# Kernel optimization log

Hardware: AMD Instinct MI355X
Metric: run time of the kernel (lower is better)

## Reference

```python
import jax, jax.numpy as jnp
import numpy as np

M, N_GRID, DIM = 32, 32, 128
N_SAMPLES = 100000


def setup_inputs() -> dict:
    key = jax.random.key(0)
    k1, k2 = jax.random.split(key)
    x = jax.random.normal(k1, (N_SAMPLES, DIM), dtype=jnp.float32)
    som_weights = jax.random.normal(k2, (M, N_GRID, DIM), dtype=jnp.float32)
    return {"x": x, "som_weights": som_weights}


def reference(x, som_weights):
    # MiniSom.activation_response([v]) puts a 1 at the best-matching unit
    # (argmin Euclidean distance over the m*n prototype grid), then flattens.
    # Batched equivalent: [N, K] squared distances -> argmin -> one-hot.
    K = som_weights.shape[0] * som_weights.shape[1]
    w = som_weights.reshape(K, -1)                       # [K, dim]
    x_sq = jnp.sum(x * x, axis=1, keepdims=True)         # [N, 1]
    w_sq = jnp.sum(w * w, axis=1)                        # [K]
    # squared Euclidean distance; argmin identical to argmin of true distance
    d2 = x_sq + w_sq[None, :] - 2.0 * (x @ w.T)          # [N, K]
    bmu = jnp.argmin(d2, axis=1)                         # [N]
    return jax.nn.one_hot(bmu, K, dtype=jnp.float32)     # [N, K]
```

## Files before the change

kernel.cpp:

```cpp
#include <hip/hip_runtime.h>


typedef __attribute__((ext_vector_type(8))) short bf16x8;
typedef __attribute__((ext_vector_type(4))) float f32x4;

#define SOM_K 1024
#define SOM_D 128
#define MARGIN 0.02f
#define FLAG_CAP 8192

#define WS_WSQ   64
#define WS_W3    8192
#define WS_FLAGS 532480

static __device__ __forceinline__ unsigned short f2bf(float f) {
    unsigned u = __float_as_uint(f);
    return (unsigned short)((u + 0x7FFFu + ((u >> 16) & 1u)) >> 16);
}
static __device__ __forceinline__ float bf2f(unsigned short h) {
    return __uint_as_float(((unsigned)h) << 16);
}

__global__ __launch_bounds__(256) void som_prep(
    const float* __restrict__ w, unsigned short* __restrict__ w3,
    float* __restrict__ wsq, int* __restrict__ flag_count)
{
    __shared__ float ws_[16][SOM_D];
    const int nt = blockIdx.x;
    const int tid = threadIdx.x;

    if (nt == 0 && tid == 0) *flag_count = 0;

    const float* src = w + (size_t)nt * 16 * SOM_D;
    #pragma unroll
    for (int r = 0; r < 8; ++r) {
        const int e = r * 256 + tid;
        ws_[e >> 7][e & 127] = src[e];
    }
    __syncthreads();

    unsigned short* dst = w3 + (size_t)nt * 4096;
    #pragma unroll
    for (int r = 0; r < 2; ++r) {
        const int G = r * 256 + tid;
        const int s = G >> 6;
        const int l = G & 63;
        const int c = l & 15, q = l >> 4;
        bf16x8 v;
        #pragma unroll
        for (int j = 0; j < 8; ++j) {
            const int kk = 32 * s + 8 * q + j;
            const int d = kk & 127;
            const float f = ws_[c][d];
            const unsigned short h = f2bf(f);
            v[j] = (short)((kk & 128) ? f2bf(f - bf2f(h)) : h);
        }
        *(bf16x8*)(dst + G * 8) = v;
    }

    if (tid < 16) {
        double s = 0.0;
        #pragma unroll 16
        for (int d = 0; d < SOM_D; ++d) {
            double v = (double)ws_[tid][d];
            s += v * v;
        }
        wsq[nt * 16 + tid] = (float)s;
    }
}

__global__ __launch_bounds__(256) void som_main(
    const float* __restrict__ x,
    const unsigned short* __restrict__ w3,
    const float* __restrict__ wsq,
    float* __restrict__ out,
    int* __restrict__ flag_count,
    int* __restrict__ flag_list,
    int n_samples)
{
    const int lane = threadIdx.x & 63;
    const int wv   = threadIdx.x >> 6;
    const int c = lane & 15;
    const int q = lane >> 4;
    const int R0 = blockIdx.x * 64 + wv * 16;

    bf16x8 ah[4], al[4];
    {
        int row = R0 + c;
        if (row >= n_samples) row = n_samples - 1;
        const float* xp = x + (size_t)row * SOM_D + 8 * q;
        #pragma unroll
        for (int s = 0; s < 4; ++s) {
            float4 v0 = *(const float4*)(xp + 32 * s);
            float4 v1 = *(const float4*)(xp + 32 * s + 4);
            float xv[8] = {v0.x, v0.y, v0.z, v0.w, v1.x, v1.y, v1.z, v1.w};
            bf16x8 hh, ll;
            #pragma unroll
            for (int j = 0; j < 8; ++j) {
                unsigned short h = f2bf(xv[j]);
                hh[j] = (short)h;
                ll[j] = (short)f2bf(xv[j] - bf2f(h));
            }
            ah[s] = hh; al[s] = ll;
        }
    }

    float best[4], sec[4];
    int bk[4];
    #pragma unroll
    for (int r = 0; r < 4; ++r) { best[r] = 1e30f; sec[r] = 1e30f; bk[r] = 0; }

    const unsigned short* wbase = w3 + lane * 8;

    #pragma unroll 1
    for (int nt = 0; nt < 64; ++nt) {
        const int n0 = nt * 16;
        const unsigned short* wp = wbase + (size_t)nt * 4096;
        bf16x8 b[8];
        #pragma unroll
        for (int s = 0; s < 8; ++s) b[s] = *(const bf16x8*)(wp + 512 * s);
        const float wq = wsq[n0 + c];

        f32x4 aA = {0.f, 0.f, 0.f, 0.f}, aB = {0.f, 0.f, 0.f, 0.f};
        #pragma unroll
        for (int s = 0; s < 4; ++s)
            aA = __builtin_amdgcn_mfma_f32_16x16x32_bf16(ah[s], b[s], aA, 0, 0, 0);
        #pragma unroll
        for (int s = 0; s < 4; ++s)
            aA = __builtin_amdgcn_mfma_f32_16x16x32_bf16(ah[s], b[4 + s], aA, 0, 0, 0);
        #pragma unroll
        for (int s = 0; s < 4; ++s)
            aB = __builtin_amdgcn_mfma_f32_16x16x32_bf16(al[s], b[s], aB, 0, 0, 0);

        #pragma unroll
        for (int r = 0; r < 4; ++r) {
            float s0 = wq - 2.f * (aA[r] + aB[r]);
            if (s0 < best[r]) { sec[r] = best[r]; best[r] = s0; bk[r] = n0 + c; }
            else if (s0 < sec[r]) sec[r] = s0;
        }
    }

    #pragma unroll
    for (int r = 0; r < 4; ++r) {
        float b0v = best[r], s0v = sec[r];
        int k0 = bk[r];
        #pragma unroll
        for (int m = 1; m < 16; m <<= 1) {
            float ob = __shfl_xor(b0v, m);
            float os = __shfl_xor(s0v, m);
            int   ok = __shfl_xor(k0, m);
            if (ob < b0v || (ob == b0v && ok < k0)) {
                s0v = fminf(b0v, os); b0v = ob; k0 = ok;
            } else {
                s0v = fminf(s0v, ob);
            }
        }
        best[r] = b0v; sec[r] = s0v; bk[r] = k0;
    }

    if (c == 0) {
        #pragma unroll
        for (int r = 0; r < 4; ++r) {
            const int row = R0 + 4 * q + r;
            if (row < n_samples && (sec[r] - best[r]) < MARGIN) {
                int i = atomicAdd(flag_count, 1);
                if (i < FLAG_CAP) flag_list[i] = row;
            }
        }
    }

    #pragma unroll 1
    for (int rr = 0; rr < 16; ++rr) {
        const int row = R0 + rr;
        if (row >= n_samples) break;
        const int b = __shfl(bk[rr & 3], (rr >> 2) << 4);
        f32x4* op = (f32x4*)(out + (size_t)row * SOM_K);
        #pragma unroll
        for (int j = 0; j < 4; ++j) {
            const int e = j * 64 + lane;
            f32x4 v = {0.f, 0.f, 0.f, 0.f};
            if ((b >> 2) == e) v[b & 3] = 1.0f;
            op[e] = v;
        }
    }
}

__global__ __launch_bounds__(1024) void som_pass2(
    const float* __restrict__ x,
    const float* __restrict__ w,
    float* __restrict__ out,
    const int* __restrict__ flag_count,
    const int* __restrict__ flag_list)
{
    __shared__ float xs[SOM_D];
    __shared__ double rbest[16];
    __shared__ int    rk[16];

    const int tid  = threadIdx.x;
    const int lane = tid & 63;
    const int wv   = tid >> 6;
    int cnt = *flag_count;
    if (cnt > FLAG_CAP) cnt = FLAG_CAP;

    for (int i = blockIdx.x; i < cnt; i += gridDim.x) {
        const int row = flag_list[i];
        __syncthreads();
        if (tid < SOM_D) xs[tid] = x[(size_t)row * SOM_D + tid];
        __syncthreads();

        const float* wk = w + (size_t)tid * SOM_D;
        double s0 = 0.0, s1 = 0.0;
        #pragma unroll
        for (int d = 0; d < SOM_D; d += 4) {
            float4 wv4 = *(const float4*)(wk + d);
            double w0 = (double)wv4.x, w1 = (double)wv4.y;
            double w2 = (double)wv4.z, w3 = (double)wv4.w;
            s0 += w0 * (w0 - 2.0 * (double)xs[d])     + w2 * (w2 - 2.0 * (double)xs[d + 2]);
            s1 += w1 * (w1 - 2.0 * (double)xs[d + 1]) + w3 * (w3 - 2.0 * (double)xs[d + 3]);
        }
        double sc = s0 + s1;
        int bk = tid;

        #pragma unroll
        for (int off = 32; off > 0; off >>= 1) {
            double os = __shfl_down(sc, off);
            int    ok = __shfl_down(bk, off);
            if (os < sc || (os == sc && ok < bk)) { sc = os; bk = ok; }
        }
        if (lane == 0) { rbest[wv] = sc; rk[wv] = bk; }
        __syncthreads();

        if (tid == 0) {
            double b = rbest[0]; int k0 = rk[0];
            #pragma unroll
            for (int v = 1; v < 16; ++v) {
                if (rbest[v] < b || (rbest[v] == b && rk[v] < k0)) { b = rbest[v]; k0 = rk[v]; }
            }
            rk[0] = k0;
        }
        __syncthreads();
        const int bmu = rk[0];

        out[(size_t)row * SOM_K + tid] = (tid == bmu) ? 1.0f : 0.0f;
    }
}

extern "C" void kernel_launch(void* const* d_in, const int* in_sizes, int n_in,
                              void* d_out, int out_size, void* d_ws, size_t ws_size,
                              hipStream_t stream) {
    const float* x = (const float*)d_in[0];
    const float* w = (const float*)d_in[1];
    float* out = (float*)d_out;

    const int n_samples = in_sizes[0] / SOM_D;

    char* ws = (char*)d_ws;
    int*            flag_count = (int*)ws;
    float*          wsq        = (float*)(ws + WS_WSQ);
    unsigned short* w3         = (unsigned short*)(ws + WS_W3);
    int*            flag_list  = (int*)(ws + WS_FLAGS);

    som_prep<<<64, 256, 0, stream>>>(w, w3, wsq, flag_count);
    const int grid = (n_samples + 63) / 64;
    som_main<<<grid, 256, 0, stream>>>(x, w3, wsq, out, flag_count, flag_list,
                                       n_samples);
    som_pass2<<<256, 1024, 0, stream>>>(x, w, out, flag_count, flag_list);
}
```

Measured before the change: 661.4 us.

## Split one-hot output writing into a separate streaming kernel after BMU refinement

New measurement: 652.2 us. About the same (-1.4%).

```diff
diff --git a/kernel.cpp b/kernel.cpp
--- a/kernel.cpp
+++ b/kernel.cpp
@@ -12,6 +12,7 @@
 #define WS_WSQ   64
 #define WS_W3    8192
 #define WS_FLAGS 532480
+#define WS_BMU   565248
 
 static __device__ __forceinline__ unsigned short f2bf(float f) {
     unsigned u = __float_as_uint(f);
@@ -73,7 +74,7 @@
     const float* __restrict__ x,
     const unsigned short* __restrict__ w3,
     const float* __restrict__ wsq,
-    float* __restrict__ out,
+    int* __restrict__ bmu_out,
     int* __restrict__ flag_count,
     int* __restrict__ flag_list,
     int n_samples)
@@ -162,25 +163,13 @@
         #pragma unroll
         for (int r = 0; r < 4; ++r) {
             const int row = R0 + 4 * q + r;
-            if (row < n_samples && (sec[r] - best[r]) < MARGIN) {
-                int i = atomicAdd(flag_count, 1);
-                if (i < FLAG_CAP) flag_list[i] = row;
-            }
-        }
-    }
-
-    #pragma unroll 1
-    for (int rr = 0; rr < 16; ++rr) {
-        const int row = R0 + rr;
-        if (row >= n_samples) break;
-        const int b = __shfl(bk[rr & 3], (rr >> 2) << 4);
-        f32x4* op = (f32x4*)(out + (size_t)row * SOM_K);
-        #pragma unroll
-        for (int j = 0; j < 4; ++j) {
-            const int e = j * 64 + lane;
-            f32x4 v = {0.f, 0.f, 0.f, 0.f};
-            if ((b >> 2) == e) v[b & 3] = 1.0f;
-            op[e] = v;
+            if (row < n_samples) {
+                bmu_out[row] = bk[r];
+                if ((sec[r] - best[r]) < MARGIN) {
+                    int i = atomicAdd(flag_count, 1);
+                    if (i < FLAG_CAP) flag_list[i] = row;
+                }
+            }
         }
     }
 }
@@ -188,7 +177,7 @@
 __global__ __launch_bounds__(1024) void som_pass2(
     const float* __restrict__ x,
     const float* __restrict__ w,
-    float* __restrict__ out,
+    int* __restrict__ bmu_out,
     const int* __restrict__ flag_count,
     const int* __restrict__ flag_list)
 {
@@ -236,12 +225,30 @@
             for (int v = 1; v < 16; ++v) {
                 if (rbest[v] < b || (rbest[v] == b && rk[v] < k0)) { b = rbest[v]; k0 = rk[v]; }
             }
-            rk[0] = k0;
-        }
-        __syncthreads();
-        const int bmu = rk[0];
-
-        out[(size_t)row * SOM_K + tid] = (tid == bmu) ? 1.0f : 0.0f;
+            bmu_out[row] = k0;
+        }
+        __syncthreads();
+    }
+}
+
+__global__ __launch_bounds__(256) void som_write(
+    float* __restrict__ out, const int* __restrict__ bmu, int n)
+{
+    const int lane = threadIdx.x & 63;
+    const int wv   = threadIdx.x >> 6;
+    int row = blockIdx.x * 4 + wv;
+    const int stride = gridDim.x * 4;
+
+    for (; row < n; row += stride) {
+        const int b = bmu[row];
+        f32x4* op = (f32x4*)(out + (size_t)row * SOM_K);
+        #pragma unroll
+        for (int j = 0; j < 4; ++j) {
+            const int e = j * 64 + lane;
+            f32x4 v = {0.f, 0.f, 0.f, 0.f};
+            if ((b >> 2) == e) v[b & 3] = 1.0f;
+            op[e] = v;
+        }
     }
 }
 
@@ -259,10 +266,12 @@
     float*          wsq        = (float*)(ws + WS_WSQ);
     unsigned short* w3         = (unsigned short*)(ws + WS_W3);
     int*            flag_list  = (int*)(ws + WS_FLAGS);
+    int*            bmu        = (int*)(ws + WS_BMU);
 
     som_prep<<<64, 256, 0, stream>>>(w, w3, wsq, flag_count);
     const int grid = (n_samples + 63) / 64;
-    som_main<<<grid, 256, 0, stream>>>(x, w3, wsq, out, flag_count, flag_list,
+    som_main<<<grid, 256, 0, stream>>>(x, w3, wsq, bmu, flag_count, flag_list,
                                        n_samples);
-    som_pass2<<<256, 1024, 0, stream>>>(x, w, out, flag_count, flag_list);
-}
+    som_pass2<<<256, 1024, 0, stream>>>(x, w, bmu, flag_count, flag_list);
+    som_write<<<1024, 256, 0, stream>>>(out, bmu, n_samples);
+}
```
